# Performance work log

Measured on AMD Instinct MI355X. Metric: run time of the kernel, lower is better.

## Reference

```python
import jax, jax.numpy as jnp
import numpy as np

B, N = 8, 2048
ZD, SD, MLP, DEPTH = 512, 64, 2048, 4


def setup_inputs() -> dict:
    key = jax.random.key(0)
    ks = jax.random.split(key, 8)
    g = lambda k, shape: jax.random.normal(k, shape, jnp.float32) * 0.02
    return {
        "z": jax.random.normal(ks[0], (B, N, ZD), jnp.float32),
        "spatial_embedding": jax.random.normal(ks[1], (B, N, SD), jnp.float32) * 0.5,
        "ln_z_scale": jnp.ones((DEPTH, ZD), jnp.float32),
        "ln_z_bias": jnp.zeros((DEPTH, ZD), jnp.float32),
        "ln_s_scale": jnp.ones((DEPTH, ZD), jnp.float32),
        "ln_s_bias": jnp.zeros((DEPTH, ZD), jnp.float32),
        "Wz1": g(ks[2], (DEPTH, ZD, MLP)), "bz1": jnp.zeros((DEPTH, MLP), jnp.float32),
        "Wz2": g(ks[3], (DEPTH, MLP, ZD)), "bz2": jnp.zeros((DEPTH, ZD), jnp.float32),
        "Ws1": g(ks[4], (DEPTH, ZD, MLP)), "bs1": jnp.zeros((DEPTH, MLP), jnp.float32),
        "Ws2": g(ks[5], (DEPTH, MLP, SD)), "bs2": jnp.zeros((DEPTH, SD), jnp.float32),
    }


def _layernorm(x, scale, bias, eps=1e-5):
    m = jnp.mean(x, axis=-1, keepdims=True)
    v = jnp.var(x, axis=-1, keepdims=True)  # biased var, matches torch LayerNorm
    return (x - m) * jax.lax.rsqrt(v + eps) * scale + bias


def _spatial_attn(e, z):
    # sim = exp(-||e_i - e_j||^2), row-normalized == softmax(-d2) over j.
    # Use |a|^2 + |b|^2 - 2ab expansion to avoid the [B,N,N,D] broadcast tensor.
    sq = jnp.sum(e * e, axis=-1)  # [B,N]
    d2 = sq[:, :, None] + sq[:, None, :] - 2.0 * jnp.einsum('bid,bjd->bij', e, e)
    d2 = jnp.maximum(d2, 0.0)
    attn = jax.nn.softmax(-d2, axis=-1)  # [B,N,N]
    return jnp.einsum('bij,bjd->bid', attn, z)


def _ff(x, W1, b1, W2, b2):
    h = jax.nn.gelu(x @ W1 + b1, approximate=False)  # torch nn.GELU() is exact erf
    return h @ W2 + b2


def reference(z, spatial_embedding, ln_z_scale, ln_z_bias, ln_s_scale, ln_s_bias,
              Wz1, bz1, Wz2, bz2, Ws1, bs1, Ws2, bs2):
    s = spatial_embedding
    for i in range(DEPTH):
        z = _spatial_attn(s, z)
        z = _ff(_layernorm(z, ln_z_scale[i], ln_z_bias[i]), Wz1[i], bz1[i], Wz2[i], bz2[i]) + z
        s = _ff(_layernorm(z, ln_s_scale[i], ln_s_bias[i]), Ws1[i], bs1[i], Ws2[i], bs2[i]) + s
    return (z, s)
```

## Files before the change

kernel.cpp:

```cpp
#include <hip/hip_runtime.h>
#include <stdint.h>

#define DEPTH 4
#define BATCH 8
#define NN 2048
#define ZDIM 512
#define SDIM 64
#define MLPD 2048
#define ROWS (BATCH*NN)

typedef __bf16 bf16x8_t __attribute__((ext_vector_type(8)));
typedef float f32x4_t __attribute__((ext_vector_type(4)));
typedef unsigned short us;

#define AS1 __attribute__((address_space(1)))
#define AS3 __attribute__((address_space(3)))

__device__ __forceinline__ void gload16(const void* g, void* l) {
  __builtin_amdgcn_global_load_lds((const AS1 void*)g, (AS3 void*)l, 16, 0, 0);
}

__device__ __forceinline__ unsigned short f2bf(float f) {
  union { float f; unsigned u; } v; v.f = f;
  unsigned u = v.u;
  unsigned r = (u + 0x7fffu + ((u >> 16) & 1u)) >> 16;
  return (unsigned short)r;
}
__device__ __forceinline__ float bf2f(unsigned short h) {
  union { unsigned u; float f; } v; v.u = ((unsigned)h) << 16;
  return v.f;
}

__device__ __forceinline__ float gelu_fast(float x) {
  float x2 = x * x;
  float q = fmaf(x2, -0.0713548162f, -1.5957691216f);
  float em = __expf(q * x);
  return x * __builtin_amdgcn_rcpf(1.0f + em);
}

#define LGKM0() do { asm volatile("s_waitcnt lgkmcnt(0)" ::: "memory"); \
                     __builtin_amdgcn_sched_barrier(0); } while (0)
#define MF(A_, B_, C_) __builtin_amdgcn_mfma_f32_16x16x32_bf16(A_, B_, C_, 0, 0, 0)

__global__ __launch_bounds__(256) void conv_e_kernel(const float* __restrict__ s,
    unsigned short* __restrict__ ebf, float* __restrict__ sq) {
  int lane = threadIdx.x & 63;
  int row = blockIdx.x * 4 + (threadIdx.x >> 6);
  float x = s[(long)row * SDIM + lane];
  unsigned short v = f2bf(x);
  ebf[(long)row * SDIM + lane] = v;
  float xb = bf2f(v);
  float ss = xb * xb;
  #pragma unroll
  for (int off = 32; off > 0; off >>= 1) ss += __shfl_xor(ss, off);
  if (lane == 0) sq[row] = ss;
}

__global__ __launch_bounds__(256) void tconv_kernel(const float* __restrict__ in,
    unsigned short* __restrict__ out, int R, int C, long sIn, long sOut) {
  __shared__ float tile[32][33];
  int b = blockIdx.z;
  int c0 = blockIdx.x * 32, r0 = blockIdx.y * 32;
  int tx = threadIdx.x, ty = threadIdx.y;
  const float* ib = in + (long)b * sIn;
  unsigned short* ob = out + (long)b * sOut;
  #pragma unroll
  for (int i = 0; i < 32; i += 8)
    tile[ty + i][tx] = ib[(long)(r0 + ty + i) * C + c0 + tx];
  __syncthreads();
  #pragma unroll
  for (int i = 0; i < 32; i += 8)
    ob[(long)(c0 + ty + i) * R + r0 + tx] = f2bf(tile[tx][ty + i]);
}

__global__ __launch_bounds__(256) void ln_kernel(const float* __restrict__ x,
    const float* __restrict__ scale, const float* __restrict__ bias,
    unsigned short* __restrict__ y) {
  int lane = threadIdx.x & 63;
  long row = (long)blockIdx.x * 4 + (threadIdx.x >> 6);
  const float* xr = x + row * ZDIM + lane * 8;
  float4 v0 = *(const float4*)xr;
  float4 v1 = *(const float4*)(xr + 4);
  float xv[8] = {v0.x, v0.y, v0.z, v0.w, v1.x, v1.y, v1.z, v1.w};
  float s1 = 0.f, s2 = 0.f;
  #pragma unroll
  for (int k = 0; k < 8; ++k) { s1 += xv[k]; s2 += xv[k] * xv[k]; }
  #pragma unroll
  for (int off = 32; off > 0; off >>= 1) {
    s1 += __shfl_xor(s1, off);
    s2 += __shfl_xor(s2, off);
  }
  float mean = s1 * (1.0f / ZDIM);
  float var = s2 * (1.0f / ZDIM) - mean * mean;
  float rstd = rsqrtf(var + 1e-5f);
  const float* sc = scale + lane * 8;
  const float* bi = bias + lane * 8;
  alignas(16) unsigned short o[8];
  #pragma unroll
  for (int k = 0; k < 8; ++k)
    o[k] = f2bf((xv[k] - mean) * rstd * sc[k] + bi[k]);
  *(uint4*)(y + row * ZDIM + lane * 8) = *(const uint4*)o;
}

__global__ __launch_bounds__(256) void attn_w_kernel(const unsigned short* __restrict__ ebf,
    const float* __restrict__ sq, unsigned short* __restrict__ wout,
    float* __restrict__ RS) {
  __shared__ unsigned short Ei[4096];
  __shared__ unsigned short Ej[8192];
  __shared__ unsigned short Wt[8192];
  int tid = threadIdx.x, lane = tid & 63, wid = tid >> 6;
  int lr = lane & 15, hi = lane >> 4;
  int q = blockIdx.y;
  int b = blockIdx.z;
  int i0 = blockIdx.x * 64;
  const unsigned short* eb = ebf + (long)b * NN * SDIM;

  int rl = tid >> 3;
  int scs = ((tid & 7) ^ (rl & 7)) * 8;
  int dstc = (tid & 192) * 8;

  #pragma unroll
  for (int it = 0; it < 2; ++it)
    gload16(eb + (long)(i0 + it * 32 + rl) * SDIM + scs, &Ei[it * 2048 + dstc]);
  #pragma unroll
  for (int it = 0; it < 4; ++it)
    gload16(eb + (long)(q * 512 + it * 32 + rl) * SDIM + scs, &Ej[it * 2048 + dstc]);
  __syncthreads();

  bf16x8_t afrag[2];
  int ka = lr & 7;
  #pragma unroll
  for (int s = 0; s < 2; ++s)
    afrag[s] = *(const bf16x8_t*)&Ei[(wid * 16 + lr) * 64 + (((s * 4 + hi) ^ ka) * 8)];
  int rloc = wid * 16 + (hi << 2);
  float sqi[4];
  #pragma unroll
  for (int r = 0; r < 4; ++r) sqi[r] = sq[b * NN + i0 + rloc + r];
  float rs[4] = {0.f, 0.f, 0.f, 0.f};
  us* stripe = &Wt[wid * 2048];

  for (int jj = 0; jj < 4; ++jj) {
    int j0 = q * 512 + jj * 128;
    if (jj > 0) {
      __syncthreads();
      #pragma unroll
      for (int it = 0; it < 4; ++it)
        gload16(eb + (long)(j0 + it * 32 + rl) * SDIM + scs, &Ej[it * 2048 + dstc]);
      __syncthreads();
    }
    #pragma unroll
    for (int n = 0; n < 8; ++n) {
      f32x4_t g = {0.f, 0.f, 0.f, 0.f};
      #pragma unroll
      for (int s = 0; s < 2; ++s) {
        int rb = n * 16 + lr;
        bf16x8_t bfr = *(const bf16x8_t*)&Ej[rb * 64 + (((s * 4 + hi) ^ (rb & 7)) * 8)];
        g = __builtin_amdgcn_mfma_f32_16x16x32_bf16(afrag[s], bfr, g, 0, 0, 0);
      }
      float sqj = sq[b * NN + j0 + n * 16 + lr];
      #pragma unroll
      for (int r = 0; r < 4; ++r) {
        float d2 = sqi[r] + sqj - 2.0f * g[r];
        d2 = fmaxf(d2, 0.0f);
        float w = __expf(-d2);
        unsigned short wb = f2bf(w);
        rs[r] += bf2f(wb);
        int srow = (hi << 2) + r;
        stripe[srow * 128 + ((n ^ (srow & 3)) * 16) + lr] = wb;
      }
    }
    LGKM0();
    #pragma unroll
    for (int it = 0; it < 4; ++it) {
      int seg = it * 64 + lane;
      int row = seg >> 4, c8 = seg & 15;
      int c8s = c8 ^ ((row & 3) << 1);
      uint4 v = *(const uint4*)&stripe[row * 128 + c8s * 8];
      long gi = i0 + wid * 16 + row;
      *(uint4*)&wout[(long)b * NN * NN + gi * NN + j0 + c8 * 8] = v;
    }
  }
  #pragma unroll
  for (int off = 1; off < 16; off <<= 1) {
    #pragma unroll
    for (int r = 0; r < 4; ++r) rs[r] += __shfl_xor(rs[r], off);
  }
  if (lr == 0) {
    #pragma unroll
    for (int r = 0; r < 4; ++r)
      RS[(long)q * ROWS + b * NN + i0 + rloc + r] = rs[r];
  }
}

__global__ __launch_bounds__(256, 4) void gemm128ff(
    const unsigned short* __restrict__ A, const unsigned short* __restrict__ BT,
    unsigned short* __restrict__ Cout, const float* __restrict__ bias,
    int Nmat, int K) {
  __shared__ unsigned short LB[16384];
  us* Asb = LB;
  us* Bsb = LB + 8192;
  int tid = threadIdx.x, lane = tid & 63;
  int lr = lane & 15, hi = lane >> 4;
  int wid = tid >> 6, wr = wid >> 1, wc = wid & 1;

  int gx = gridDim.x;
  int wg = blockIdx.y * gx + blockIdx.x;
  int nwg = gx * gridDim.y;
  if ((nwg & 7) == 0) wg = (wg & 7) * (nwg >> 3) + (wg >> 3);
  int bj = wg % gx, bi = wg / gx;
  int row0 = bi * 128, col0 = bj * 128;

  int rl = tid >> 3;
  int scs = ((tid & 7) ^ (rl & 7)) * 8;
  const unsigned short* pA[4];
  const unsigned short* pB[4];
  #pragma unroll
  for (int it = 0; it < 4; ++it) {
    pA[it] = A + (long)(row0 + it * 32 + rl) * K + scs;
    pB[it] = BT + (long)(col0 + it * 32 + rl) * K + scs;
  }
  int dstc = (tid & 192) * 8;

  int offA[4][2], offB[4][2];
  #pragma unroll
  for (int m = 0; m < 4; ++m) {
    #pragma unroll
    for (int s = 0; s < 2; ++s) {
      int ra = wr * 64 + m * 16 + lr;
      offA[m][s] = ra * 64 + (((s * 4 + hi) ^ (ra & 7)) * 8);
      int rb = wc * 64 + m * 16 + lr;
      offB[m][s] = rb * 64 + (((s * 4 + hi) ^ (rb & 7)) * 8);
    }
  }

  auto stage = [&]() {
    #pragma unroll
    for (int it = 0; it < 4; ++it) { gload16(pA[it], &Asb[it * 2048 + dstc]); pA[it] += 64; }
    #pragma unroll
    for (int it = 0; it < 4; ++it) { gload16(pB[it], &Bsb[it * 2048 + dstc]); pB[it] += 64; }
  };

  f32x4_t acc[4][4];
  #pragma unroll
  for (int m = 0; m < 4; ++m)
    #pragma unroll
    for (int n = 0; n < 4; ++n) acc[m][n] = (f32x4_t){0.f, 0.f, 0.f, 0.f};

  int nk = K >> 6;
  stage();

  for (int t = 0; t < nk; ++t) {
    __syncthreads();
    bf16x8_t a0[4], b0[4];
    #pragma unroll
    for (int m = 0; m < 4; ++m) a0[m] = *(const bf16x8_t*)&Asb[offA[m][0]];
    #pragma unroll
    for (int n = 0; n < 4; ++n) b0[n] = *(const bf16x8_t*)&Bsb[offB[n][0]];
    #pragma unroll
    for (int m = 0; m < 4; ++m)
      #pragma unroll
      for (int n = 0; n < 4; ++n)
        acc[m][n] = MF(a0[m], b0[n], acc[m][n]);
    bf16x8_t a1[4], b1[4];
    #pragma unroll
    for (int m = 0; m < 4; ++m) a1[m] = *(const bf16x8_t*)&Asb[offA[m][1]];
    #pragma unroll
    for (int n = 0; n < 4; ++n) b1[n] = *(const bf16x8_t*)&Bsb[offB[n][1]];
    __syncthreads();
    if (t + 1 < nk) stage();
    #pragma unroll
    for (int m = 0; m < 4; ++m)
      #pragma unroll
      for (int n = 0; n < 4; ++n)
        acc[m][n] = MF(a1[m], b1[n], acc[m][n]);
  }

  int cbase = col0 + wc * 64 + lr;
  float bv[4];
  #pragma unroll
  for (int n = 0; n < 4; ++n) bv[n] = bias[cbase + n * 16];
  us* stripe = LB + wid * 4096;
  #pragma unroll
  for (int m = 0; m < 4; ++m) {
    #pragma unroll
    for (int r = 0; r < 4; ++r) {
      int sr = m * 16 + hi * 4 + r;
      #pragma unroll
      for (int n = 0; n < 4; ++n)
        stripe[sr * 64 + ((n ^ (sr & 3)) * 16) + lr] =
            f2bf(gelu_fast(acc[m][n][r] + bv[n]));
    }
  }
  LGKM0();
  #pragma unroll
  for (int it = 0; it < 8; ++it) {
    int seg = it * 64 + lane;
    int sr = seg >> 3, c8 = seg & 7;
    int c8s = c8 ^ ((sr & 3) << 1);
    uint4 v = *(const uint4*)&stripe[sr * 64 + c8s * 8];
    long row = row0 + wr * 64 + sr;
    *(uint4*)&Cout[row * Nmat + col0 + wc * 64 + c8 * 8] = v;
  }
}

template <int EPI>
__global__ __launch_bounds__(256, 4) void gemm128g(
    const unsigned short* __restrict__ A, const unsigned short* __restrict__ BT,
    float* __restrict__ Cout, const float* __restrict__ bias,
    const float* __restrict__ resid, const float* __restrict__ RS,
    int Nmat, int K, long sA, long sB, long sC, long sR) {
  __shared__ unsigned short LB[16384];
  us* Asb = LB;
  us* Bsb = LB + 8192;
  int tid = threadIdx.x, lane = tid & 63;
  int lr = lane & 15, hi = lane >> 4;
  int wid = tid >> 6, wr = wid >> 1, wc = wid & 1;
  int bb = blockIdx.z;

  int gx = gridDim.x;
  int wg = blockIdx.y * gx + blockIdx.x;
  int nwg = gx * gridDim.y;
  if ((nwg & 7) == 0) wg = (wg & 7) * (nwg >> 3) + (wg >> 3);
  int bj = wg % gx, bi = wg / gx;
  int row0 = bi * 128, col0 = bj * 128;

  const unsigned short* Ab = A + (long)bb * sA;
  const unsigned short* Bb = BT + (long)bb * sB;

  int rl = tid >> 3;
  int scs = ((tid & 7) ^ (rl & 7)) * 8;
  const unsigned short* pA[4];
  const unsigned short* pB[4];
  #pragma unroll
  for (int it = 0; it < 4; ++it) {
    pA[it] = Ab + (long)(row0 + it * 32 + rl) * K + scs;
    pB[it] = Bb + (long)(col0 + it * 32 + rl) * K + scs;
  }
  int dstc = (tid & 192) * 8;

  int offA[4][2], offB[4][2];
  #pragma unroll
  for (int m = 0; m < 4; ++m) {
    #pragma unroll
    for (int s = 0; s < 2; ++s) {
      int ra = wr * 64 + m * 16 + lr;
      offA[m][s] = ra * 64 + (((s * 4 + hi) ^ (ra & 7)) * 8);
      int rb = wc * 64 + m * 16 + lr;
      offB[m][s] = rb * 64 + (((s * 4 + hi) ^ (rb & 7)) * 8);
    }
  }

  auto stage = [&]() {
    #pragma unroll
    for (int it = 0; it < 4; ++it) { gload16(pA[it], &Asb[it * 2048 + dstc]); pA[it] += 64; }
    #pragma unroll
    for (int it = 0; it < 4; ++it) { gload16(pB[it], &Bsb[it * 2048 + dstc]); pB[it] += 64; }
  };

  f32x4_t acc[4][4];
  #pragma unroll
  for (int m = 0; m < 4; ++m)
    #pragma unroll
    for (int n = 0; n < 4; ++n) acc[m][n] = (f32x4_t){0.f, 0.f, 0.f, 0.f};

  int nk = K >> 6;
  stage();

  for (int t = 0; t < nk; ++t) {
    __syncthreads();
    bf16x8_t a0[4], b0[4];
    #pragma unroll
    for (int m = 0; m < 4; ++m) a0[m] = *(const bf16x8_t*)&Asb[offA[m][0]];
    #pragma unroll
    for (int n = 0; n < 4; ++n) b0[n] = *(const bf16x8_t*)&Bsb[offB[n][0]];
    #pragma unroll
    for (int m = 0; m < 4; ++m)
      #pragma unroll
      for (int n = 0; n < 4; ++n)
        acc[m][n] = MF(a0[m], b0[n], acc[m][n]);
    bf16x8_t a1[4], b1[4];
    #pragma unroll
    for (int m = 0; m < 4; ++m) a1[m] = *(const bf16x8_t*)&Asb[offA[m][1]];
    #pragma unroll
    for (int n = 0; n < 4; ++n) b1[n] = *(const bf16x8_t*)&Bsb[offB[n][1]];
    __syncthreads();
    if (t + 1 < nk) stage();
    #pragma unroll
    for (int m = 0; m < 4; ++m)
      #pragma unroll
      for (int n = 0; n < 4; ++n)
        acc[m][n] = MF(a1[m], b1[n], acc[m][n]);
  }

  int rbase = row0 + wr * 64 + hi * 4;
  int cbase = col0 + wc * 64 + lr;
  float bv[4];
  #pragma unroll
  for (int n = 0; n < 4; ++n) bv[n] = (EPI == 2) ? bias[cbase + n * 16] : 0.f;
  #pragma unroll
  for (int m = 0; m < 4; ++m) {
    #pragma unroll
    for (int r = 0; r < 4; ++r) {
      int row = rbase + m * 16 + r;
      float ir = 0.f;
      if (EPI == 0) {
        long idx = (long)bb * sR + row;
        float den = RS[idx] + RS[ROWS + idx] + RS[2L * ROWS + idx] + RS[3L * ROWS + idx];
        ir = 1.0f / den;
      }
      #pragma unroll
      for (int n = 0; n < 4; ++n) {
        int col = cbase + n * 16;
        long cidx = (long)bb * sC + (long)row * Nmat + col;
        if (EPI == 0) {
          Cout[cidx] = acc[m][n][r] * ir;
        } else {
          Cout[cidx] = acc[m][n][r] + bv[n] + resid[(long)bb * sR + (long)row * Nmat + col];
        }
      }
    }
  }
}

template <int EPI>
__global__ __launch_bounds__(256, 4) void gemm3b(
    const unsigned short* __restrict__ A, const unsigned short* __restrict__ BT,
    void* __restrict__ Cout, const float* __restrict__ bias,
    const float* __restrict__ resid, const float* __restrict__ RS,
    int Nmat, int K, long sA, long sB, long sC, long sR) {
  __shared__ unsigned short As[64 * 64];
  __shared__ unsigned short Bs[128 * 64];
  int tid = threadIdx.x, lane = tid & 63;
  int lr = lane & 15, hi = lane >> 4;
  int wid = tid >> 6, wr = wid >> 1, wc = wid & 1;
  int bb = blockIdx.z;

  int gx = gridDim.x;
  int wg = blockIdx.y * gx + blockIdx.x;
  int nwg = gx * gridDim.y;
  if ((nwg & 7) == 0) wg = (wg & 7) * (nwg >> 3) + (wg >> 3);
  int bj = wg % gx, bi = wg / gx;
  int row0 = bi * 64, col0 = bj * 128;

  const unsigned short* Ab = A + (long)bb * sA;
  const unsigned short* Bb = BT + (long)bb * sB;

  int rl = tid >> 3;
  int scs = ((tid & 7) ^ (rl & 7)) * 8;
  const unsigned short* pA[2];
  const unsigned short* pB[4];
  #pragma unroll
  for (int it = 0; it < 2; ++it)
    pA[it] = Ab + (long)(row0 + it * 32 + rl) * K + scs;
  #pragma unroll
  for (int it = 0; it < 4; ++it) {
    int rb = col0 + it * 32 + rl;
    if (rb > Nmat - 1) rb = Nmat - 1;
    pB[it] = Bb + (long)rb * K + scs;
  }
  int dstc = (tid & 192) * 8;

  int offA[2][2], offB[4][2];
  #pragma unroll
  for (int m = 0; m < 2; ++m)
    #pragma unroll
    for (int s = 0; s < 2; ++s) {
      int ra = wr * 32 + m * 16 + lr;
      offA[m][s] = ra * 64 + (((s * 4 + hi) ^ (ra & 7)) * 8);
    }
  #pragma unroll
  for (int n = 0; n < 4; ++n)
    #pragma unroll
    for (int s = 0; s < 2; ++s) {
      int rb = wc * 64 + n * 16 + lr;
      offB[n][s] = rb * 64 + (((s * 4 + hi) ^ (rb & 7)) * 8);
    }

  auto stage = [&]() {
    #pragma unroll
    for (int it = 0; it < 2; ++it) { gload16(pA[it], &As[it * 2048 + dstc]); pA[it] += 64; }
    #pragma unroll
    for (int it = 0; it < 4; ++it) { gload16(pB[it], &Bs[it * 2048 + dstc]); pB[it] += 64; }
  };

  f32x4_t acc[2][4];
  #pragma unroll
  for (int m = 0; m < 2; ++m)
    #pragma unroll
    for (int n = 0; n < 4; ++n) acc[m][n] = (f32x4_t){0.f, 0.f, 0.f, 0.f};

  int nk = K >> 6;
  stage();

  for (int t = 0; t < nk; ++t) {
    __syncthreads();
    bf16x8_t a0s0 = *(const bf16x8_t*)&As[offA[0][0]];
    bf16x8_t a1s0 = *(const bf16x8_t*)&As[offA[1][0]];
    bf16x8_t a0s1 = *(const bf16x8_t*)&As[offA[0][1]];
    bf16x8_t a1s1 = *(const bf16x8_t*)&As[offA[1][1]];
    bf16x8_t b0s0 = *(const bf16x8_t*)&Bs[offB[0][0]];
    bf16x8_t b1s0 = *(const bf16x8_t*)&Bs[offB[1][0]];
    bf16x8_t b2s0 = *(const bf16x8_t*)&Bs[offB[2][0]];
    bf16x8_t b3s0 = *(const bf16x8_t*)&Bs[offB[3][0]];
    bf16x8_t b0s1 = *(const bf16x8_t*)&Bs[offB[0][1]];
    bf16x8_t b1s1 = *(const bf16x8_t*)&Bs[offB[1][1]];
    bf16x8_t b2s1 = *(const bf16x8_t*)&Bs[offB[2][1]];
    bf16x8_t b3s1 = *(const bf16x8_t*)&Bs[offB[3][1]];
    __syncthreads();
    if (t + 1 < nk) stage();
    acc[0][0] = MF(a0s0, b0s0, acc[0][0]);
    acc[1][0] = MF(a1s0, b0s0, acc[1][0]);
    acc[0][1] = MF(a0s0, b1s0, acc[0][1]);
    acc[1][1] = MF(a1s0, b1s0, acc[1][1]);
    acc[0][2] = MF(a0s0, b2s0, acc[0][2]);
    acc[1][2] = MF(a1s0, b2s0, acc[1][2]);
    acc[0][3] = MF(a0s0, b3s0, acc[0][3]);
    acc[1][3] = MF(a1s0, b3s0, acc[1][3]);
    acc[0][0] = MF(a0s1, b0s1, acc[0][0]);
    acc[1][0] = MF(a1s1, b0s1, acc[1][0]);
    acc[0][1] = MF(a0s1, b1s1, acc[0][1]);
    acc[1][1] = MF(a1s1, b1s1, acc[1][1]);
    acc[0][2] = MF(a0s1, b2s1, acc[0][2]);
    acc[1][2] = MF(a1s1, b2s1, acc[1][2]);
    acc[0][3] = MF(a0s1, b3s1, acc[0][3]);
    acc[1][3] = MF(a1s1, b3s1, acc[1][3]);
  }

  int rbase = row0 + wr * 32 + hi * 4;
  int cbase = col0 + wc * 64 + lr;
  #pragma unroll
  for (int m = 0; m < 2; ++m) {
    #pragma unroll
    for (int r = 0; r < 4; ++r) {
      int row = rbase + m * 16 + r;
      #pragma unroll
      for (int n = 0; n < 4; ++n) {
        int col = cbase + n * 16;
        if (col >= Nmat) continue;
        float v = acc[m][n][r];
        long cidx = (long)bb * sC + (long)row * Nmat + col;
        ((float*)Cout)[cidx] = v + bias[col] + resid[(long)bb * sR + (long)row * Nmat + col];
      }
    }
  }
}

extern "C" void kernel_launch(void* const* d_in, const int* in_sizes, int n_in,
                              void* d_out, int out_size, void* d_ws, size_t ws_size,
                              hipStream_t stream) {
  (void)in_sizes; (void)n_in; (void)out_size; (void)ws_size;
  const float* in_z   = (const float*)d_in[0];
  const float* in_s   = (const float*)d_in[1];
  const float* lnz_sc = (const float*)d_in[2];
  const float* lnz_bi = (const float*)d_in[3];
  const float* lns_sc = (const float*)d_in[4];
  const float* lns_bi = (const float*)d_in[5];
  const float* Wz1 = (const float*)d_in[6];
  const float* bz1 = (const float*)d_in[7];
  const float* Wz2 = (const float*)d_in[8];
  const float* bz2 = (const float*)d_in[9];
  const float* Ws1 = (const float*)d_in[10];
  const float* bs1 = (const float*)d_in[11];
  const float* Ws2 = (const float*)d_in[12];
  const float* bs2 = (const float*)d_in[13];
  float* out_z = (float*)d_out;
  float* out_s = out_z + (long)ROWS * ZDIM;

  char* ws = (char*)d_ws;
  size_t off = 0;
  auto alloc = [&](size_t bytes) { void* p = ws + off; off += (bytes + 255) & ~(size_t)255; return p; };
  unsigned short* WH   = (unsigned short*)alloc((size_t)BATCH * NN * NN * 2);
  unsigned short* ZT   = (unsigned short*)alloc((size_t)BATCH * ZDIM * NN * 2);
  unsigned short* XLN  = (unsigned short*)alloc((size_t)ROWS * ZDIM * 2);
  unsigned short* EBF  = (unsigned short*)alloc((size_t)ROWS * SDIM * 2);
  float* ZATT = (float*)alloc((size_t)ROWS * ZDIM * 4);
  float* ZBUF = (float*)alloc((size_t)ROWS * ZDIM * 4);
  float* SBUF = (float*)alloc((size_t)ROWS * SDIM * 4);
  float* SQ   = (float*)alloc((size_t)ROWS * 4);
  float* RS   = (float*)alloc((size_t)4 * ROWS * 4);
  unsigned short* W1Z = (unsigned short*)alloc((size_t)DEPTH * MLPD * ZDIM * 2);
  unsigned short* W2Z = (unsigned short*)alloc((size_t)DEPTH * ZDIM * MLPD * 2);
  unsigned short* W1S = (unsigned short*)alloc((size_t)DEPTH * MLPD * ZDIM * 2);
  unsigned short* W2S = (unsigned short*)alloc((size_t)DEPTH * SDIM * MLPD * 2);

  tconv_kernel<<<dim3(MLPD / 32, ZDIM / 32, DEPTH), dim3(32, 8), 0, stream>>>(
      Wz1, W1Z, ZDIM, MLPD, (long)ZDIM * MLPD, (long)MLPD * ZDIM);
  tconv_kernel<<<dim3(ZDIM / 32, MLPD / 32, DEPTH), dim3(32, 8), 0, stream>>>(
      Wz2, W2Z, MLPD, ZDIM, (long)MLPD * ZDIM, (long)ZDIM * MLPD);
  tconv_kernel<<<dim3(MLPD / 32, ZDIM / 32, DEPTH), dim3(32, 8), 0, stream>>>(
      Ws1, W1S, ZDIM, MLPD, (long)ZDIM * MLPD, (long)MLPD * ZDIM);
  tconv_kernel<<<dim3(SDIM / 32, MLPD / 32, DEPTH), dim3(32, 8), 0, stream>>>(
      Ws2, W2S, MLPD, SDIM, (long)MLPD * SDIM, (long)SDIM * MLPD);

  for (int L = 0; L < DEPTH; ++L) {
    const float* z_in = (L == 0) ? in_z : ZBUF;
    const float* s_in = (L == 0) ? in_s : SBUF;
    float* z_out = (L == DEPTH - 1) ? out_z : ZBUF;
    float* s_out = (L == DEPTH - 1) ? out_s : SBUF;

    conv_e_kernel<<<ROWS / 4, 256, 0, stream>>>(s_in, EBF, SQ);
    tconv_kernel<<<dim3(ZDIM / 32, NN / 32, BATCH), dim3(32, 8), 0, stream>>>(
        z_in, ZT, NN, ZDIM, (long)NN * ZDIM, (long)ZDIM * NN);
    attn_w_kernel<<<dim3(NN / 64, 4, BATCH), 256, 0, stream>>>(EBF, SQ, WH, RS);
    gemm128g<0><<<dim3(ZDIM / 128, NN / 128, BATCH), 256, 0, stream>>>(
        WH, ZT, ZATT, nullptr, nullptr, RS,
        ZDIM, NN, (long)NN * NN, (long)ZDIM * NN, (long)NN * ZDIM, NN);
    ln_kernel<<<ROWS / 4, 256, 0, stream>>>(ZATT, lnz_sc + L * ZDIM, lnz_bi + L * ZDIM, XLN);
    gemm128ff<<<dim3(MLPD / 128, ROWS / 128, 1), 256, 0, stream>>>(
        XLN, W1Z + (long)L * MLPD * ZDIM, WH, bz1 + L * MLPD, MLPD, ZDIM);
    gemm128g<2><<<dim3(ZDIM / 128, ROWS / 128, 1), 256, 0, stream>>>(
        WH, W2Z + (long)L * ZDIM * MLPD, z_out, bz2 + L * ZDIM, ZATT, nullptr,
        ZDIM, MLPD, 0, 0, 0, 0);
    ln_kernel<<<ROWS / 4, 256, 0, stream>>>(z_out, lns_sc + L * ZDIM, lns_bi + L * ZDIM, XLN);
    gemm128ff<<<dim3(MLPD / 128, ROWS / 128, 1), 256, 0, stream>>>(
        XLN, W1S + (long)L * MLPD * ZDIM, WH, bs1 + L * MLPD, MLPD, ZDIM);
    gemm3b<2><<<dim3(1, ROWS / 64, 1), 256, 0, stream>>>(
        WH, W2S + (long)L * SDIM * MLPD, s_out, bs2 + L * SDIM, s_in, nullptr,
        SDIM, MLPD, 0, 0, 0, 0);
  }
}
```

Before: 979.7 us.

## Split attention-weight kernel over more j-chunks and use split-K for the s-FFN output GEMM

```diff
diff --git a/kernel.cpp b/kernel.cpp
--- a/kernel.cpp
+++ b/kernel.cpp
@@ -124,7 +124,7 @@
     gload16(eb + (long)(i0 + it * 32 + rl) * SDIM + scs, &Ei[it * 2048 + dstc]);
   #pragma unroll
   for (int it = 0; it < 4; ++it)
-    gload16(eb + (long)(q * 512 + it * 32 + rl) * SDIM + scs, &Ej[it * 2048 + dstc]);
+    gload16(eb + (long)(q * 256 + it * 32 + rl) * SDIM + scs, &Ej[it * 2048 + dstc]);
   __syncthreads();
 
   bf16x8_t afrag[2];
@@ -139,8 +139,8 @@
   float rs[4] = {0.f, 0.f, 0.f, 0.f};
   us* stripe = &Wt[wid * 2048];
 
-  for (int jj = 0; jj < 4; ++jj) {
-    int j0 = q * 512 + jj * 128;
+  for (int jj = 0; jj < 2; ++jj) {
+    int j0 = q * 256 + jj * 128;
     if (jj > 0) {
       __syncthreads();
       #pragma unroll
@@ -405,7 +405,9 @@
       float ir = 0.f;
       if (EPI == 0) {
         long idx = (long)bb * sR + row;
-        float den = RS[idx] + RS[ROWS + idx] + RS[2L * ROWS + idx] + RS[3L * ROWS + idx];
+        float den = 0.f;
+        #pragma unroll
+        for (int qq = 0; qq < 8; ++qq) den += RS[(long)qq * ROWS + idx];
         ir = 1.0f / den;
       }
       #pragma unroll
@@ -422,42 +424,28 @@
   }
 }
 
-template <int EPI>
-__global__ __launch_bounds__(256, 4) void gemm3b(
+__global__ __launch_bounds__(256, 4) void ff2s_part(
     const unsigned short* __restrict__ A, const unsigned short* __restrict__ BT,
-    void* __restrict__ Cout, const float* __restrict__ bias,
-    const float* __restrict__ resid, const float* __restrict__ RS,
-    int Nmat, int K, long sA, long sB, long sC, long sR) {
-  __shared__ unsigned short As[64 * 64];
-  __shared__ unsigned short Bs[128 * 64];
+    float* __restrict__ SPART, int K) {
+  __shared__ unsigned short As[128 * 64];
+  __shared__ unsigned short Bs[64 * 64];
   int tid = threadIdx.x, lane = tid & 63;
   int lr = lane & 15, hi = lane >> 4;
-  int wid = tid >> 6, wr = wid >> 1, wc = wid & 1;
-  int bb = blockIdx.z;
-
-  int gx = gridDim.x;
-  int wg = blockIdx.y * gx + blockIdx.x;
-  int nwg = gx * gridDim.y;
-  if ((nwg & 7) == 0) wg = (wg & 7) * (nwg >> 3) + (wg >> 3);
-  int bj = wg % gx, bi = wg / gx;
-  int row0 = bi * 64, col0 = bj * 128;
-
-  const unsigned short* Ab = A + (long)bb * sA;
-  const unsigned short* Bb = BT + (long)bb * sB;
+  int wid = tid >> 6;
+  int kz = blockIdx.z;
+  int row0 = blockIdx.y * 128;
 
   int rl = tid >> 3;
   int scs = ((tid & 7) ^ (rl & 7)) * 8;
-  const unsigned short* pA[2];
-  const unsigned short* pB[4];
+  long kbase = (long)kz * 512;
+  const unsigned short* pA[4];
+  #pragma unroll
+  for (int it = 0; it < 4; ++it)
+    pA[it] = A + (long)(row0 + it * 32 + rl) * K + kbase + scs;
+  const unsigned short* pB[2];
   #pragma unroll
   for (int it = 0; it < 2; ++it)
-    pA[it] = Ab + (long)(row0 + it * 32 + rl) * K + scs;
-  #pragma unroll
-  for (int it = 0; it < 4; ++it) {
-    int rb = col0 + it * 32 + rl;
-    if (rb > Nmat - 1) rb = Nmat - 1;
-    pB[it] = Bb + (long)rb * K + scs;
-  }
+    pB[it] = BT + (long)(it * 32 + rl) * K + kbase + scs;
   int dstc = (tid & 192) * 8;
 
   int offA[2][2], offB[4][2];
@@ -465,22 +453,22 @@
   for (int m = 0; m < 2; ++m)
     #pragma unroll
     for (int s = 0; s < 2; ++s) {
-      int ra = wr * 32 + m * 16 + lr;
+      int ra = wid * 32 + m * 16 + lr;
       offA[m][s] = ra * 64 + (((s * 4 + hi) ^ (ra & 7)) * 8);
     }
   #pragma unroll
   for (int n = 0; n < 4; ++n)
     #pragma unroll
     for (int s = 0; s < 2; ++s) {
-      int rb = wc * 64 + n * 16 + lr;
+      int rb = n * 16 + lr;
       offB[n][s] = rb * 64 + (((s * 4 + hi) ^ (rb & 7)) * 8);
     }
 
   auto stage = [&]() {
     #pragma unroll
-    for (int it = 0; it < 2; ++it) { gload16(pA[it], &As[it * 2048 + dstc]); pA[it] += 64; }
-    #pragma unroll
-    for (int it = 0; it < 4; ++it) { gload16(pB[it], &Bs[it * 2048 + dstc]); pB[it] += 64; }
+    for (int it = 0; it < 4; ++it) { gload16(pA[it], &As[it * 2048 + dstc]); pA[it] += 64; }
+    #pragma unroll
+    for (int it = 0; it < 2; ++it) { gload16(pB[it], &Bs[it * 2048 + dstc]); pB[it] += 64; }
   };
 
   f32x4_t acc[2][4];
@@ -489,10 +477,8 @@
     #pragma unroll
     for (int n = 0; n < 4; ++n) acc[m][n] = (f32x4_t){0.f, 0.f, 0.f, 0.f};
 
-  int nk = K >> 6;
   stage();
-
-  for (int t = 0; t < nk; ++t) {
+  for (int t = 0; t < 8; ++t) {
     __syncthreads();
     bf16x8_t a0s0 = *(const bf16x8_t*)&As[offA[0][0]];
     bf16x8_t a1s0 = *(const bf16x8_t*)&As[offA[1][0]];
@@ -507,7 +493,7 @@
     bf16x8_t b2s1 = *(const bf16x8_t*)&Bs[offB[2][1]];
     bf16x8_t b3s1 = *(const bf16x8_t*)&Bs[offB[3][1]];
     __syncthreads();
-    if (t + 1 < nk) stage();
+    if (t + 1 < 8) stage();
     acc[0][0] = MF(a0s0, b0s0, acc[0][0]);
     acc[1][0] = MF(a1s0, b0s0, acc[1][0]);
     acc[0][1] = MF(a0s0, b1s0, acc[0][1]);
@@ -526,23 +512,27 @@
     acc[1][3] = MF(a1s1, b3s1, acc[1][3]);
   }
 
-  int rbase = row0 + wr * 32 + hi * 4;
-  int cbase = col0 + wc * 64 + lr;
+  float* outp = SPART + (long)kz * ROWS * SDIM;
   #pragma unroll
   for (int m = 0; m < 2; ++m) {
     #pragma unroll
     for (int r = 0; r < 4; ++r) {
-      int row = rbase + m * 16 + r;
-      #pragma unroll
-      for (int n = 0; n < 4; ++n) {
-        int col = cbase + n * 16;
-        if (col >= Nmat) continue;
-        float v = acc[m][n][r];
-        long cidx = (long)bb * sC + (long)row * Nmat + col;
-        ((float*)Cout)[cidx] = v + bias[col] + resid[(long)bb * sR + (long)row * Nmat + col];
-      }
-    }
-  }
+      int row = row0 + wid * 32 + m * 16 + hi * 4 + r;
+      #pragma unroll
+      for (int n = 0; n < 4; ++n)
+        outp[(long)row * SDIM + n * 16 + lr] = acc[m][n][r];
+    }
+  }
+}
+
+__global__ __launch_bounds__(256) void ff2s_red(const float* __restrict__ SPART,
+    const float* __restrict__ bias, const float* __restrict__ resid,
+    float* __restrict__ out) {
+  long idx = (long)blockIdx.x * 256 + threadIdx.x;
+  int col = idx & (SDIM - 1);
+  float v = SPART[idx] + SPART[(long)ROWS * SDIM + idx] +
+            SPART[2L * ROWS * SDIM + idx] + SPART[3L * ROWS * SDIM + idx];
+  out[idx] = v + bias[col] + resid[idx];
 }
 
 extern "C" void kernel_launch(void* const* d_in, const int* in_sizes, int n_in,
@@ -577,7 +567,8 @@
   float* ZBUF = (float*)alloc((size_t)ROWS * ZDIM * 4);
   float* SBUF = (float*)alloc((size_t)ROWS * SDIM * 4);
   float* SQ   = (float*)alloc((size_t)ROWS * 4);
-  float* RS   = (float*)alloc((size_t)4 * ROWS * 4);
+  float* RS   = (float*)alloc((size_t)8 * ROWS * 4);
+  float* SPART = (float*)alloc((size_t)4 * ROWS * SDIM * 4);
   unsigned short* W1Z = (unsigned short*)alloc((size_t)DEPTH * MLPD * ZDIM * 2);
   unsigned short* W2Z = (unsigned short*)alloc((size_t)DEPTH * ZDIM * MLPD * 2);
   unsigned short* W1S = (unsigned short*)alloc((size_t)DEPTH * MLPD * ZDIM * 2);
@@ -601,7 +592,7 @@
     conv_e_kernel<<<ROWS / 4, 256, 0, stream>>>(s_in, EBF, SQ);
     tconv_kernel<<<dim3(ZDIM / 32, NN / 32, BATCH), dim3(32, 8), 0, stream>>>(
         z_in, ZT, NN, ZDIM, (long)NN * ZDIM, (long)ZDIM * NN);
-    attn_w_kernel<<<dim3(NN / 64, 4, BATCH), 256, 0, stream>>>(EBF, SQ, WH, RS);
+    attn_w_kernel<<<dim3(NN / 64, 8, BATCH), 256, 0, stream>>>(EBF, SQ, WH, RS);
     gemm128g<0><<<dim3(ZDIM / 128, NN / 128, BATCH), 256, 0, stream>>>(
         WH, ZT, ZATT, nullptr, nullptr, RS,
         ZDIM, NN, (long)NN * NN, (long)ZDIM * NN, (long)NN * ZDIM, NN);
@@ -614,8 +605,9 @@
     ln_kernel<<<ROWS / 4, 256, 0, stream>>>(z_out, lns_sc + L * ZDIM, lns_bi + L * ZDIM, XLN);
     gemm128ff<<<dim3(MLPD / 128, ROWS / 128, 1), 256, 0, stream>>>(
         XLN, W1S + (long)L * MLPD * ZDIM, WH, bs1 + L * MLPD, MLPD, ZDIM);
-    gemm3b<2><<<dim3(1, ROWS / 64, 1), 256, 0, stream>>>(
-        WH, W2S + (long)L * SDIM * MLPD, s_out, bs2 + L * SDIM, s_in, nullptr,
-        SDIM, MLPD, 0, 0, 0, 0);
-  }
-}
+    ff2s_part<<<dim3(1, ROWS / 128, 4), 256, 0, stream>>>(
+        WH, W2S + (long)L * SDIM * MLPD, SPART, MLPD);
+    ff2s_red<<<ROWS * SDIM / 256, 256, 0, stream>>>(
+        SPART, bs2 + L * SDIM, s_in, s_out);
+  }
+}
```

Result: faster. 942.6 us, median of 2 (-3.8%).
